# Kernel optimization log

Measured on AMD Instinct MI355X. Metric: run time of the kernel, lower is better.

Reference implementation:

```python
import jax, jax.numpy as jnp
import numpy as np

N_WIRES = 8
DIM = 2 ** N_WIRES  # 256
NUM_HEADS = 4

def _cnot_ring_perm():
    # Compose CNOT(w, w+1) for w=0..6 then CNOT(7, 0) into one basis permutation.
    # Wire 0 is the most-significant bit of the basis index.
    perm = np.arange(DIM)
    pairs = [(w, w + 1) for w in range(N_WIRES - 1)] + [(N_WIRES - 1, 0)]
    j = np.arange(DIM)
    for c, t in pairs:
        ctrl = (j >> (N_WIRES - 1 - c)) & 1
        M = j ^ (ctrl << (N_WIRES - 1 - t))  # flip target bit where control=1 (involution)
        perm = perm[M]
    return perm

PERM = _cnot_ring_perm()
# SIGNS[i, w] = <i|Z_w|i> = 1 - 2*bit_w(i)
SIGNS = np.array([[1.0 - 2.0 * ((i >> (N_WIRES - 1 - w)) & 1) for w in range(N_WIRES)]
                  for i in range(DIM)], dtype=np.float32)

def setup_inputs() -> dict:
    key = jax.random.key(0)
    k1, k2, k3 = jax.random.split(key, 3)
    x = jax.random.normal(k1, (16, 4096, N_WIRES), jnp.float32)  # rotation angles per token
    theta = jax.random.normal(k2, (N_WIRES,), jnp.float32)       # trainable RX params
    w_combine = jax.random.normal(k3, (N_WIRES, N_WIRES), jnp.float32) / np.float32(np.sqrt(N_WIRES))
    b_combine = jnp.zeros((N_WIRES,), jnp.float32)
    return {"x": x, "theta": theta, "w_combine": w_combine, "b_combine": b_combine}

def _quantum_features(x, theta):
    # RX(x_i) then RX(theta_i) on wire i compose to RX(x_i + theta_i) acting on |0>.
    B, S, E = x.shape
    N = B * S
    phi = (x + theta).reshape(N, E)
    c = jnp.cos(0.5 * phi).astype(jnp.complex64)
    s = (-1j) * jnp.sin(0.5 * phi)          # RX|0> = cos(phi/2)|0> - i sin(phi/2)|1>
    wv = jnp.stack([c, s.astype(jnp.complex64)], axis=-1)  # (N, 8, 2)
    # Build product state via successive Kronecker products (wire 0 = MSB).
    state = jnp.ones((N, 1), jnp.complex64)
    for w in range(E):
        state = (state[:, :, None] * wv[:, w, None, :]).reshape(N, -1)  # (N, 2^(w+1))
    state = state[:, jnp.asarray(PERM)]      # apply the CNOT ring as one permutation
    probs = state.real ** 2 + state.imag ** 2  # (N, 256)
    return (probs @ jnp.asarray(SIGNS)).reshape(B, S, E)  # <Z_w> per token

def reference(x, theta, w_combine, b_combine):
    B, S, E = x.shape
    d_k = E // NUM_HEADS
    q = _quantum_features(x, theta)           # (B, S, 8); k = v = q in the source
    scores = jnp.einsum('bse,bte->bst', q, q) / np.float32(np.sqrt(d_k))
    attn = jax.nn.softmax(scores, axis=-1)    # dropout is identity in eval mode
    out = jnp.einsum('bst,bte->bse', attn, q)
    # Faithful to source: transpose(1,2).contiguous().view(B, S, E)
    out = jnp.swapaxes(out, 1, 2).reshape(B, S, E)
    return out @ w_combine.T + b_combine
```

## Files before the change

### kernel.cpp

```cpp
#include <hip/hip_runtime.h>
#include <math.h>


#define SEQ   4096
#define NB    16
#define SROWS 128
#define TPB   1024
#define NTG   4
#define TC    512
#define NCH   (SEQ / TC)
#define TPT   4
#define KSTR  12
#define VSTR  520
#define KFSZ  (TC * KSTR)
#define VTSZ  (9 * VSTR)

typedef _Float16 f16x4  __attribute__((ext_vector_type(4)));
typedef _Float16 f16x8  __attribute__((ext_vector_type(8)));
typedef float    f32x16 __attribute__((ext_vector_type(16)));
typedef __fp16   hf2    __attribute__((ext_vector_type(2)));

#if __has_builtin(__builtin_amdgcn_exp2f)
#define EXP2F(x) __builtin_amdgcn_exp2f(x)
#else
#define EXP2F(x) exp2f(x)
#endif

__global__ __launch_bounds__(TPB, 8)
void qattn_kernel(const float* __restrict__ x, const float* __restrict__ theta,
                  const float* __restrict__ wc, const float* __restrict__ bc,
                  float* __restrict__ out)
{
    __shared__ __align__(16) _Float16 kf[2 * KFSZ];
    __shared__ __align__(16) _Float16 vt[2 * VTSZ];
    float* part = (float*)kf;
    float* attn = (float*)vt;

    const int tid  = threadIdx.x;
    const int lane = tid & 63;
    const int wv   = tid >> 6;
    const int sub  = wv & 3;
    const int tg   = wv >> 2;
    const int l31  = lane & 31;
    const int hp   = lane >> 5;

    const int b  = blockIdx.x >> 5;
    const int S0 = (blockIdx.x & 31) * SROWS;
    const float* xb = x + (size_t)b * SEQ * 8;

    const int pos = (tid & ~12) | ((tid & 4) << 1) | ((tid & 8) >> 1);

    float th[8];
#pragma unroll
    for (int w = 0; w < 8; ++w) th[w] = theta[w];

    f16x4 qfrag;
    {
        const int s = S0 + sub * 32 + l31;
        const float4 xa  = *(const float4*)(xb + s * 8);
        const float4 xb4 = *(const float4*)(xb + s * 8 + 4);
        float c0 = __cosf(xa.x  + th[0]);
        float c1 = __cosf(xa.y  + th[1]);
        float c2 = __cosf(xa.z  + th[2]);
        float c3 = __cosf(xa.w  + th[3]);
        float c4 = __cosf(xb4.x + th[4]);
        float c5 = __cosf(xb4.y + th[5]);
        float c6 = __cosf(xb4.z + th[6]);
        float c7 = __cosf(xb4.w + th[7]);
        float p1 = c0 * c1, p2 = p1 * c2, p3 = p2 * c3, p4 = p3 * c4;
        float p5 = p4 * c5, p6 = p5 * c6, p7 = p6 * c7;
        float p0 = c1 * c2 * c3 * c4 * c5 * c6 * c7;
        const float sc = 0.70710678118654752f * 1.44269504088896341f;
        if (hp == 0)
            qfrag = (f16x4){(_Float16)(p0*sc), (_Float16)(p1*sc),
                            (_Float16)(p2*sc), (_Float16)(p3*sc)};
        else
            qfrag = (f16x4){(_Float16)(p4*sc), (_Float16)(p5*sc),
                            (_Float16)(p6*sc), (_Float16)(p7*sc)};
    }

    auto mkrow = [&](int tt, f16x4& r0, f16x4& r1) {
        const float4 xa  = *(const float4*)(xb + tt * 8);
        const float4 xb4 = *(const float4*)(xb + tt * 8 + 4);
        float c0 = __cosf(xa.x  + th[0]);
        float c1 = __cosf(xa.y  + th[1]);
        float c2 = __cosf(xa.z  + th[2]);
        float c3 = __cosf(xa.w  + th[3]);
        float c4 = __cosf(xb4.x + th[4]);
        float c5 = __cosf(xb4.y + th[5]);
        float c6 = __cosf(xb4.z + th[6]);
        float c7 = __cosf(xb4.w + th[7]);
        float p1 = c0 * c1, p2 = p1 * c2, p3 = p2 * c3, p4 = p3 * c4;
        float p5 = p4 * c5, p6 = p5 * c6, p7 = p6 * c7;
        float p0 = c1 * c2 * c3 * c4 * c5 * c6 * c7;
        r0 = (f16x4){(_Float16)p0, (_Float16)p1, (_Float16)p2, (_Float16)p3};
        r1 = (f16x4){(_Float16)p4, (_Float16)p5, (_Float16)p6, (_Float16)p7};
    };
    auto dswr = [&](int buf, f16x4 r0, f16x4 r1) {
        _Float16* krow = kf + buf * KFSZ + tid * KSTR;
        *(f16x4*)(krow)     = r0;
        *(f16x4*)(krow + 4) = r1;
        _Float16* vb = vt + buf * VTSZ + pos;
        vb[0 * VSTR] = r0[0];
        vb[1 * VSTR] = r0[1];
        vb[2 * VSTR] = r0[2];
        vb[3 * VSTR] = r0[3];
        vb[4 * VSTR] = r1[0];
        vb[5 * VSTR] = r1[1];
        vb[6 * VSTR] = r1[2];
        vb[7 * VSTR] = r1[3];
    };

    f16x4 hc0, hc1;
    if (tid < TC) {
        vt[0 * VTSZ + 8 * VSTR + tid] = (_Float16)1.0f;
        vt[1 * VTSZ + 8 * VSTR + tid] = (_Float16)1.0f;
        f16x4 a0, a1;
        mkrow(tid, a0, a1);
        dswr(0, a0, a1);
        mkrow(TC + tid, hc0, hc1);
    }

    f32x16 o = {0.f,0.f,0.f,0.f,0.f,0.f,0.f,0.f,0.f,0.f,0.f,0.f,0.f,0.f,0.f,0.f};
    const f32x16 zc = (f32x16){0.f,0.f,0.f,0.f,0.f,0.f,0.f,0.f,
                               0.f,0.f,0.f,0.f,0.f,0.f,0.f,0.f};

    const int wr = (l31 < 8) ? l31 : 8;
    __syncthreads();

    for (int ch = 0; ch < NCH; ++ch) {
        const int c = ch & 1;
        if (ch + 1 < NCH && tid < TC) {
            dswr(c ^ 1, hc0, hc1);
        }
        if (ch + 2 < NCH && tid < TC) {
            mkrow((ch + 2) * TC + tid, hc0, hc1);
        }
        const _Float16* kfb = kf + c * KFSZ + l31 * KSTR + 4 * hp + tg * (TPT * 32) * KSTR;
        const _Float16* vbb = vt + c * VTSZ + wr * VSTR + 8 * hp + tg * (TPT * 32);
#pragma unroll
        for (int i = 0; i < TPT; ++i) {
            f16x4 kfrag = *(const f16x4*)(kfb + i * 32 * KSTR);
            f32x16 cc = __builtin_amdgcn_mfma_f32_32x32x8f16(kfrag, qfrag, zc, 0, 0, 0);
#pragma unroll
            for (int h = 0; h < 2; ++h) {
                union { hf2 q[4]; f16x8 v; } pa;
                pa.q[0] = __builtin_amdgcn_cvt_pkrtz(EXP2F(cc[8*h+0]), EXP2F(cc[8*h+1]));
                pa.q[1] = __builtin_amdgcn_cvt_pkrtz(EXP2F(cc[8*h+2]), EXP2F(cc[8*h+3]));
                pa.q[2] = __builtin_amdgcn_cvt_pkrtz(EXP2F(cc[8*h+4]), EXP2F(cc[8*h+5]));
                pa.q[3] = __builtin_amdgcn_cvt_pkrtz(EXP2F(cc[8*h+6]), EXP2F(cc[8*h+7]));
                f16x8 vfrag = *(const f16x8*)(vbb + i * 32 + h * 16);
                o = __builtin_amdgcn_mfma_f32_32x32x16_f16(pa.v, vfrag, o, 0, 0, 0);
            }
        }
        __syncthreads();
    }

    if (l31 < 9) {
#pragma unroll
        for (int r = 0; r < 16; ++r) {
            const int sloc = sub * 32 + (r & 3) + 8 * (r >> 2) + 4 * hp;
            part[((tg * SROWS) + sloc) * 9 + l31] = o[r];
        }
    }
    __syncthreads();
    for (int idx = tid; idx < SROWS * 9; idx += TPB) {
        const int rr = idx / 9;
        const int w  = idx - rr * 9;
        float sm = 0.f;
#pragma unroll
        for (int g = 0; g < NTG; ++g) sm += part[((g * SROWS) + rr) * 9 + w];
        attn[rr * 9 + w] = sm;
    }
    __syncthreads();
    if (tid < SROWS * 8) {
        const int rr = tid >> 3;
        const int w  = tid & 7;
        attn[rr * 9 + w] = attn[rr * 9 + w] / attn[rr * 9 + 8];
    }
    __syncthreads();

    if (tid < SROWS) {
        const int e    = tid >> 4;
        const int nloc = tid & 15;
        const int r    = e * 512 + (S0 >> 3) + nloc;
        float y[8];
#pragma unroll
        for (int c = 0; c < 8; ++c) y[c] = attn[(nloc * 8 + c) * 9 + e];
        float oo[8];
#pragma unroll
        for (int k = 0; k < 8; ++k) {
            float a = bc[k];
#pragma unroll
            for (int c = 0; c < 8; ++c) a += y[c] * wc[k * 8 + c];
            oo[k] = a;
        }
        float4* op = (float4*)(out + ((size_t)b * SEQ + r) * 8);
        op[0] = make_float4(oo[0], oo[1], oo[2], oo[3]);
        op[1] = make_float4(oo[4], oo[5], oo[6], oo[7]);
    }
}

extern "C" void kernel_launch(void* const* d_in, const int* in_sizes, int n_in,
                              void* d_out, int out_size, void* d_ws, size_t ws_size,
                              hipStream_t stream)
{
    const float* x  = (const float*)d_in[0];
    const float* th = (const float*)d_in[1];
    const float* wc = (const float*)d_in[2];
    const float* bc = (const float*)d_in[3];
    float* out = (float*)d_out;

    qattn_kernel<<<dim3(NB * (SEQ / SROWS)), dim3(TPB), 0, stream>>>(x, th, wc, bc, out);
}
```

Before: 88.93 us.

## Precompute quantum features once in a separate kernel and stream fp16 rows

```diff
diff --git a/kernel.cpp b/kernel.cpp
--- a/kernel.cpp
+++ b/kernel.cpp
@@ -14,6 +14,7 @@
 #define VSTR  520
 #define KFSZ  (TC * KSTR)
 #define VTSZ  (9 * VSTR)
+#define QTPB  256
 
 typedef _Float16 f16x4  __attribute__((ext_vector_type(4)));
 typedef _Float16 f16x8  __attribute__((ext_vector_type(8)));
@@ -26,8 +27,40 @@
 #define EXP2F(x) exp2f(x)
 #endif
 
+__global__ __launch_bounds__(QTPB)
+void qgen_kernel(const float* __restrict__ x, const float* __restrict__ theta,
+                 _Float16* __restrict__ qg, _Float16* __restrict__ qs)
+{
+    const int n = blockIdx.x * QTPB + threadIdx.x;
+    float th[8];
+#pragma unroll
+    for (int w = 0; w < 8; ++w) th[w] = theta[w];
+    const float4 xa  = *(const float4*)(x + (size_t)n * 8);
+    const float4 xb4 = *(const float4*)(x + (size_t)n * 8 + 4);
+    float c0 = __cosf(xa.x  + th[0]);
+    float c1 = __cosf(xa.y  + th[1]);
+    float c2 = __cosf(xa.z  + th[2]);
+    float c3 = __cosf(xa.w  + th[3]);
+    float c4 = __cosf(xb4.x + th[4]);
+    float c5 = __cosf(xb4.y + th[5]);
+    float c6 = __cosf(xb4.z + th[6]);
+    float c7 = __cosf(xb4.w + th[7]);
+    float p1 = c0 * c1, p2 = p1 * c2, p3 = p2 * c3, p4 = p3 * c4;
+    float p5 = p4 * c5, p6 = p5 * c6, p7 = p6 * c7;
+    float p0 = c1 * c2 * c3 * c4 * c5 * c6 * c7;
+    const float sc = 0.70710678118654752f * 1.44269504088896341f;
+    f16x8 u = (f16x8){(_Float16)p0, (_Float16)p1, (_Float16)p2, (_Float16)p3,
+                      (_Float16)p4, (_Float16)p5, (_Float16)p6, (_Float16)p7};
+    f16x8 v = (f16x8){(_Float16)(p0*sc), (_Float16)(p1*sc),
+                      (_Float16)(p2*sc), (_Float16)(p3*sc),
+                      (_Float16)(p4*sc), (_Float16)(p5*sc),
+                      (_Float16)(p6*sc), (_Float16)(p7*sc)};
+    *(f16x8*)(qg + (size_t)n * 8) = u;
+    *(f16x8*)(qs + (size_t)n * 8) = v;
+}
+
 __global__ __launch_bounds__(TPB, 8)
-void qattn_kernel(const float* __restrict__ x, const float* __restrict__ theta,
+void qattn_kernel(const _Float16* __restrict__ qg, const _Float16* __restrict__ qs,
                   const float* __restrict__ wc, const float* __restrict__ bc,
                   float* __restrict__ out)
 {
@@ -46,79 +79,37 @@
 
     const int b  = blockIdx.x >> 5;
     const int S0 = (blockIdx.x & 31) * SROWS;
-    const float* xb = x + (size_t)b * SEQ * 8;
+    const _Float16* qbg = qg + (size_t)b * SEQ * 8;
 
     const int pos = (tid & ~12) | ((tid & 4) << 1) | ((tid & 8) >> 1);
-
-    float th[8];
-#pragma unroll
-    for (int w = 0; w < 8; ++w) th[w] = theta[w];
 
     f16x4 qfrag;
     {
         const int s = S0 + sub * 32 + l31;
-        const float4 xa  = *(const float4*)(xb + s * 8);
-        const float4 xb4 = *(const float4*)(xb + s * 8 + 4);
-        float c0 = __cosf(xa.x  + th[0]);
-        float c1 = __cosf(xa.y  + th[1]);
-        float c2 = __cosf(xa.z  + th[2]);
-        float c3 = __cosf(xa.w  + th[3]);
-        float c4 = __cosf(xb4.x + th[4]);
-        float c5 = __cosf(xb4.y + th[5]);
-        float c6 = __cosf(xb4.z + th[6]);
-        float c7 = __cosf(xb4.w + th[7]);
-        float p1 = c0 * c1, p2 = p1 * c2, p3 = p2 * c3, p4 = p3 * c4;
-        float p5 = p4 * c5, p6 = p5 * c6, p7 = p6 * c7;
-        float p0 = c1 * c2 * c3 * c4 * c5 * c6 * c7;
-        const float sc = 0.70710678118654752f * 1.44269504088896341f;
-        if (hp == 0)
-            qfrag = (f16x4){(_Float16)(p0*sc), (_Float16)(p1*sc),
-                            (_Float16)(p2*sc), (_Float16)(p3*sc)};
-        else
-            qfrag = (f16x4){(_Float16)(p4*sc), (_Float16)(p5*sc),
-                            (_Float16)(p6*sc), (_Float16)(p7*sc)};
-    }
-
-    auto mkrow = [&](int tt, f16x4& r0, f16x4& r1) {
-        const float4 xa  = *(const float4*)(xb + tt * 8);
-        const float4 xb4 = *(const float4*)(xb + tt * 8 + 4);
-        float c0 = __cosf(xa.x  + th[0]);
-        float c1 = __cosf(xa.y  + th[1]);
-        float c2 = __cosf(xa.z  + th[2]);
-        float c3 = __cosf(xa.w  + th[3]);
-        float c4 = __cosf(xb4.x + th[4]);
-        float c5 = __cosf(xb4.y + th[5]);
-        float c6 = __cosf(xb4.z + th[6]);
-        float c7 = __cosf(xb4.w + th[7]);
-        float p1 = c0 * c1, p2 = p1 * c2, p3 = p2 * c3, p4 = p3 * c4;
-        float p5 = p4 * c5, p6 = p5 * c6, p7 = p6 * c7;
-        float p0 = c1 * c2 * c3 * c4 * c5 * c6 * c7;
-        r0 = (f16x4){(_Float16)p0, (_Float16)p1, (_Float16)p2, (_Float16)p3};
-        r1 = (f16x4){(_Float16)p4, (_Float16)p5, (_Float16)p6, (_Float16)p7};
+        qfrag = *(const f16x4*)(qs + ((size_t)b * SEQ + s) * 8 + 4 * hp);
+    }
+
+    auto dswr = [&](int buf, f16x8 h) {
+        _Float16* krow = kf + buf * KFSZ + tid * KSTR;
+        *(f16x4*)(krow)     = (f16x4){h[0], h[1], h[2], h[3]};
+        *(f16x4*)(krow + 4) = (f16x4){h[4], h[5], h[6], h[7]};
+        _Float16* vb = vt + buf * VTSZ + pos;
+        vb[0 * VSTR] = h[0];
+        vb[1 * VSTR] = h[1];
+        vb[2 * VSTR] = h[2];
+        vb[3 * VSTR] = h[3];
+        vb[4 * VSTR] = h[4];
+        vb[5 * VSTR] = h[5];
+        vb[6 * VSTR] = h[6];
+        vb[7 * VSTR] = h[7];
     };
-    auto dswr = [&](int buf, f16x4 r0, f16x4 r1) {
-        _Float16* krow = kf + buf * KFSZ + tid * KSTR;
-        *(f16x4*)(krow)     = r0;
-        *(f16x4*)(krow + 4) = r1;
-        _Float16* vb = vt + buf * VTSZ + pos;
-        vb[0 * VSTR] = r0[0];
-        vb[1 * VSTR] = r0[1];
-        vb[2 * VSTR] = r0[2];
-        vb[3 * VSTR] = r0[3];
-        vb[4 * VSTR] = r1[0];
-        vb[5 * VSTR] = r1[1];
-        vb[6 * VSTR] = r1[2];
-        vb[7 * VSTR] = r1[3];
-    };
-
-    f16x4 hc0, hc1;
+
+    f16x8 hq;
     if (tid < TC) {
         vt[0 * VTSZ + 8 * VSTR + tid] = (_Float16)1.0f;
         vt[1 * VTSZ + 8 * VSTR + tid] = (_Float16)1.0f;
-        f16x4 a0, a1;
-        mkrow(tid, a0, a1);
-        dswr(0, a0, a1);
-        mkrow(TC + tid, hc0, hc1);
+        dswr(0, *(const f16x8*)(qbg + (size_t)tid * 8));
+        hq = *(const f16x8*)(qbg + (size_t)(TC + tid) * 8);
     }
 
     f32x16 o = {0.f,0.f,0.f,0.f,0.f,0.f,0.f,0.f,0.f,0.f,0.f,0.f,0.f,0.f,0.f,0.f};
@@ -131,10 +122,10 @@
     for (int ch = 0; ch < NCH; ++ch) {
         const int c = ch & 1;
         if (ch + 1 < NCH && tid < TC) {
-            dswr(c ^ 1, hc0, hc1);
+            dswr(c ^ 1, hq);
         }
         if (ch + 2 < NCH && tid < TC) {
-            mkrow((ch + 2) * TC + tid, hc0, hc1);
+            hq = *(const f16x8*)(qbg + (size_t)((ch + 2) * TC + tid) * 8);
         }
         const _Float16* kfb = kf + c * KFSZ + l31 * KSTR + 4 * hp + tg * (TPT * 32) * KSTR;
         const _Float16* vbb = vt + c * VTSZ + wr * VSTR + 8 * hp + tg * (TPT * 32);
@@ -211,5 +202,9 @@
     const float* bc = (const float*)d_in[3];
     float* out = (float*)d_out;
 
-    qattn_kernel<<<dim3(NB * (SEQ / SROWS)), dim3(TPB), 0, stream>>>(x, th, wc, bc, out);
+    _Float16* qg = (_Float16*)d_ws;
+    _Float16* qs = qg + (size_t)NB * SEQ * 8;
+
+    qgen_kernel<<<dim3(NB * SEQ / QTPB), dim3(QTPB), 0, stream>>>(x, th, qg, qs);
+    qattn_kernel<<<dim3(NB * (SEQ / SROWS)), dim3(TPB), 0, stream>>>(qg, qs, wc, bc, out);
 }
```

Result: no change. 88.92 us (-0.0%).
